# Kernel tuning notes

Hardware: AMD Instinct MI355X
Metric: run time of the kernel (lower is better)

Reference implementation:

```python
import jax, jax.numpy as jnp
import numpy as np

EPS = 1e-5
NEG = -10000.0


def rel_shift(x):
    # x: [B, H, T1, T2] with T2 = 2*T1 - 1 -> returns [B, H, T1, T1]
    B, H, T1, T2 = x.shape
    x = jnp.pad(x, ((0, 0), (0, 0), (0, 0), (1, 0)))        # [B,H,T1,T2+1]
    x = x.reshape(B, H, T2 + 1, T1)[:, :, 1:, :].reshape(B, H, T1, T2)
    return x[:, :, :, : T2 // 2 + 1]


def setup_inputs() -> dict:
    key = jax.random.key(0)
    B, C, T, H = 4, 512, 1024, 8
    ks = jax.random.split(key, 16)
    s = 0.02
    inp = {
        "x": jax.random.normal(ks[0], (B, C, T), jnp.float32),
        "pos_emb": jax.random.normal(ks[1], (1, C, 2 * T - 1), jnp.float32),
        "x_mask": jnp.ones((B, 1, T), jnp.float32),
        "gamma": jnp.ones((C,), jnp.float32),
        "beta": jnp.zeros((C,), jnp.float32),
        "Wq": jax.random.normal(ks[2], (C, C), jnp.float32) * s,
        "bq": jnp.zeros((C,), jnp.float32),
        "Wk": jax.random.normal(ks[3], (C, C), jnp.float32) * s,
        "bk": jnp.zeros((C,), jnp.float32),
        "Wv": jax.random.normal(ks[4], (C, C), jnp.float32) * s,
        "bv": jnp.zeros((C,), jnp.float32),
        "Wp": jax.random.normal(ks[5], (C, C), jnp.float32) * s,
        "u_bias": jax.random.normal(ks[6], (H, C // H), jnp.float32) * s,
        "v_bias": jax.random.normal(ks[7], (H, C // H), jnp.float32) * s,
        "Wo": jax.random.normal(ks[8], (C, C), jnp.float32) * s,
        "bo": jnp.zeros((C,), jnp.float32),
    }
    return inp


def reference(x, pos_emb, x_mask, gamma, beta, Wq, bq, Wk, bk, Wv, bv, Wp,
              u_bias, v_bias, Wo, bo):
    B, C, T = x.shape
    H, Dh = u_bias.shape

    # channel LayerNorm (axis=1)
    mean = jnp.mean(x, axis=1, keepdims=True)
    var = jnp.mean((x - mean) ** 2, axis=1, keepdims=True)
    xn = (x - mean) * jax.lax.rsqrt(var + EPS)
    xn = xn * gamma[None, :, None] + beta[None, :, None]

    conv1x1 = lambda W, b, z: jnp.einsum('oc,bct->bot', W, z) + b[None, :, None]
    q = conv1x1(Wq, bq, xn).reshape(B, H, Dh, T)
    k = conv1x1(Wk, bk, xn).reshape(B, H, Dh, T)
    v = conv1x1(Wv, bv, xn).reshape(B, H, Dh, T)
    p = jnp.einsum('oc,xct->xot', Wp, pos_emb)          # [1, C, 2T-1], no bias
    p = p.reshape(p.shape[0], H, Dh, -1)[0]             # [H, Dh, 2T-1]

    content = jnp.einsum('bhdt,bhds->bhts', q + u_bias[None, :, :, None], k)
    pos = jnp.einsum('bhdt,hds->bhts', q + v_bias[None, :, :, None], p)
    pos = rel_shift(pos)                                 # [B, H, T, T]

    score = (content + pos) / jnp.sqrt(jnp.float32(C))
    attn_mask = x_mask[:, :, None, :] * x_mask[:, :, :, None]  # [B,1,T,T]
    score = jnp.where(attn_mask == 0, NEG, score)
    attn = jax.nn.softmax(score, axis=-1)

    # context[d,t] = sum_s v[d,s] * attn[s,t]
    ctx = jnp.einsum('bhds,bhst->bhdt', v, attn).reshape(B, C, T)
    return jnp.einsum('oc,bct->bot', Wo, ctx) + bo[None, :, None]
```

## Files before the change

kernel.cpp:

```cpp
#include <hip/hip_runtime.h>
#include <hip/hip_bf16.h>
#include <cmath>

typedef unsigned short u16;
typedef __bf16 bf16_t;
typedef bf16_t bf16x8 __attribute__((ext_vector_type(8)));
typedef float f32x4 __attribute__((ext_vector_type(4)));
typedef u16 u16x8 __attribute__((ext_vector_type(8)));

#define MFMA16(A,B,C) __builtin_amdgcn_mfma_f32_16x16x32_bf16(A,B,C,0,0,0)

#define CB 512
#define TT 1024
#define NH 8
#define DH 64
#define ALPHA (0.044194173824159216f * 1.4426950408889634f)
#define MASKL 14426.950408889634f

static __device__ __forceinline__ u16 f2b(float f) {
  unsigned u = __float_as_uint(f);
  unsigned r = u + 0x7FFFu + ((u >> 16) & 1u);
  return (u16)(r >> 16);
}
static __device__ __forceinline__ float b2f(u16 u) {
  return __uint_as_float(((unsigned)u) << 16);
}
static __device__ __forceinline__ bf16x8 ldb8(const u16* p) {
  return *reinterpret_cast<const bf16x8*>(p);
}

__global__ __launch_bounds__(256)
void convert5(const float* __restrict__ Wq, const float* __restrict__ Wk,
              const float* __restrict__ Wv, const float* __restrict__ Wp,
              const float* __restrict__ Wo,
              u16* __restrict__ Wstk, u16* __restrict__ WoB)
{
  int i = blockIdx.x * 256 + threadIdx.x;
  int sel = i >> 15, loc = i & 32767;
  const float* src = (sel == 0) ? Wq : (sel == 1) ? Wk : (sel == 2) ? Wv
                   : (sel == 3) ? Wp : Wo;
  const float4 a = ((const float4*)src)[loc * 2 + 0];
  const float4 b = ((const float4*)src)[loc * 2 + 1];
  u16x8 o;
  o[0] = f2b(a.x); o[1] = f2b(a.y); o[2] = f2b(a.z); o[3] = f2b(a.w);
  o[4] = f2b(b.x); o[5] = f2b(b.y); o[6] = f2b(b.z); o[7] = f2b(b.w);
  u16* dst = (sel < 4) ? (Wstk + (size_t)i * 8) : (WoB + (size_t)loc * 8);
  *(u16x8*)dst = o;
}

__global__ __launch_bounds__(256)
void transpose_pe(const float* __restrict__ pe, u16* __restrict__ posT)
{
  __shared__ float tile[64][65];
  int j0 = blockIdx.x * 64, c0 = blockIdx.y * 64;
  for (int e = threadIdx.x; e < 4096; e += 256) {
    int cc = e >> 6, jj = e & 63;
    int j = j0 + jj;
    tile[jj][cc] = (j < 2047) ? pe[(size_t)(c0 + cc) * 2047 + j] : 0.f;
  }
  __syncthreads();
  for (int e = threadIdx.x; e < 4096; e += 256) {
    int jj = e >> 6, cc = e & 63;
    posT[(size_t)(j0 + jj) * 512 + c0 + cc] = f2b(tile[jj][cc]);
  }
}

__global__ __launch_bounds__(256)
void ln_kernel(const float* __restrict__ x, const float* __restrict__ gamma,
               const float* __restrict__ beta, u16* __restrict__ xnT)
{
  __shared__ float sred[8][33], ssred[8][33];
  int tl = threadIdx.x & 31, cg = threadIdx.x >> 5;
  int t = blockIdx.x * 32 + tl;
  int b = blockIdx.y;
  const float* xb = x + (size_t)b * CB * TT + t;
  float s = 0.f, ss = 0.f;
  for (int c = cg * 64; c < cg * 64 + 64; ++c) {
    float v = xb[(size_t)c * TT];
    s += v; ss += v * v;
  }
  sred[cg][tl] = s; ssred[cg][tl] = ss;
  __syncthreads();
  float S = 0.f, SS = 0.f;
  #pragma unroll
  for (int g = 0; g < 8; ++g) { S += sred[g][tl]; SS += ssred[g][tl]; }
  float mean = S * (1.f / 512.f);
  float var = SS * (1.f / 512.f) - mean * mean;
  float rstd = rsqrtf(var + 1e-5f);
  u16* orow = xnT + ((size_t)b * TT + t) * CB;
  for (int c8 = 0; c8 < 8; ++c8) {
    int c = cg * 64 + c8 * 8;
    u16x8 o;
    #pragma unroll
    for (int j = 0; j < 8; ++j) {
      float v = xb[(size_t)(c + j) * TT];
      o[j] = f2b((v - mean) * rstd * gamma[c + j] + beta[c + j]);
    }
    *(u16x8*)(orow + c) = o;
  }
}

template<int K, int OMODE>
__global__ __launch_bounds__(256)
void gemm2(const u16* __restrict__ A, const u16* __restrict__ XT,
           long xStride, long oStride, int Nout,
           const float* __restrict__ b0, void* __restrict__ outv)
{
  const int tid = threadIdx.x, w = tid >> 6, lane = tid & 63;
  const int ln16 = lane & 15, kg = lane >> 4;
  const int wm = w & 1, wn = w >> 1;
  const int m0 = blockIdx.y * 64 + wm * 32;
  const int n0 = blockIdx.x * 128 + wn * 64;
  const int z = blockIdx.z;
  const u16* Ar = A + (size_t)(m0 + ln16) * K + kg * 8;
  const u16* Br = XT + (size_t)z * xStride + (size_t)(n0 + ln16) * K + kg * 8;
  f32x4 acc[2][4] = {};
  #pragma unroll 2
  for (int ks = 0; ks < K / 32; ++ks) {
    bf16x8 a[2], bb[4];
    #pragma unroll
    for (int mt = 0; mt < 2; ++mt) a[mt] = ldb8(Ar + (size_t)mt * 16 * K + ks * 32);
    #pragma unroll
    for (int nt = 0; nt < 4; ++nt) bb[nt] = ldb8(Br + (size_t)nt * 16 * K + ks * 32);
    #pragma unroll
    for (int mt = 0; mt < 2; ++mt)
      #pragma unroll
      for (int nt = 0; nt < 4; ++nt)
        acc[mt][nt] = MFMA16(a[mt], bb[nt], acc[mt][nt]);
  }
  float add[2][4];
  #pragma unroll
  for (int mt = 0; mt < 2; ++mt)
    #pragma unroll
    for (int jr = 0; jr < 4; ++jr)
      add[mt][jr] = b0 ? b0[m0 + mt * 16 + kg * 4 + jr] : 0.f;
  #pragma unroll
  for (int mt = 0; mt < 2; ++mt)
    #pragma unroll
    for (int nt = 0; nt < 4; ++nt) {
      const int n = n0 + nt * 16 + ln16;
      if constexpr (OMODE == 0) {
        float* out = (float*)outv;
        #pragma unroll
        for (int jr = 0; jr < 4; ++jr)
          out[(size_t)z * oStride + (size_t)(m0 + mt * 16 + kg * 4 + jr) * Nout + n] =
              acc[mt][nt][jr] + add[mt][jr];
      } else {
        const int m_low = m0 + mt * 16;
        const size_t o = (size_t)z * oStride +
                         ((size_t)(m_low >> 6) * Nout + n) * 64 + (m_low & 63) + kg * 4;
        ushort4 s4;
        s4.x = f2b(acc[mt][nt][0] + add[mt][0]);
        s4.y = f2b(acc[mt][nt][1] + add[mt][1]);
        s4.z = f2b(acc[mt][nt][2] + add[mt][2]);
        s4.w = f2b(acc[mt][nt][3] + add[mt][3]);
        *reinterpret_cast<ushort4*>((u16*)outv + o) = s4;
      }
    }
}

__global__ __launch_bounds__(256)
void proj_qkv2(const u16* __restrict__ Wstk, const u16* __restrict__ xnT,
               const float* __restrict__ bq, const float* __restrict__ ub,
               const float* __restrict__ bk, const float* __restrict__ bv,
               u16* __restrict__ quB, u16* __restrict__ kB, u16* __restrict__ vB)
{
  const int tid = threadIdx.x, w = tid >> 6, lane = tid & 63;
  const int ln16 = lane & 15, kg = lane >> 4;
  const int wm = w & 1, wn = w >> 1;
  const int my = blockIdx.y;
  const int sec = my >> 3;
  const int m0l = (my & 7) * 64 + wm * 32;
  const int n0 = blockIdx.x * 128 + wn * 64;
  const int z = blockIdx.z;
  const long XS = (long)TT * CB;
  const long QS = (long)NH * TT * DH;
  const u16* Ar = Wstk + (size_t)(sec * 512 + m0l + ln16) * 512 + kg * 8;
  const u16* Br = xnT + (size_t)z * XS + (size_t)(n0 + ln16) * 512 + kg * 8;
  f32x4 acc[2][4] = {};
  #pragma unroll 2
  for (int ks = 0; ks < 16; ++ks) {
    bf16x8 a[2], bb[4];
    #pragma unroll
    for (int mt = 0; mt < 2; ++mt) a[mt] = ldb8(Ar + (size_t)mt * 16 * 512 + ks * 32);
    #pragma unroll
    for (int nt = 0; nt < 4; ++nt) bb[nt] = ldb8(Br + (size_t)nt * 16 * 512 + ks * 32);
    #pragma unroll
    for (int mt = 0; mt < 2; ++mt)
      #pragma unroll
      for (int nt = 0; nt < 4; ++nt)
        acc[mt][nt] = MFMA16(a[mt], bb[nt], acc[mt][nt]);
  }
  const float scl = (sec == 0) ? ALPHA : 1.f;
  float add[2][4];
  #pragma unroll
  for (int mt = 0; mt < 2; ++mt)
    #pragma unroll
    for (int jr = 0; jr < 4; ++jr) {
      int m = m0l + mt * 16 + kg * 4 + jr;
      add[mt][jr] = (sec == 0) ? (bq[m] + ub[m]) : (sec == 1) ? bk[m] : bv[m];
    }
  if (sec < 2) {
    u16* dst = sec ? kB : quB;
    #pragma unroll
    for (int mt = 0; mt < 2; ++mt)
      #pragma unroll
      for (int nt = 0; nt < 4; ++nt) {
        const int n = n0 + nt * 16 + ln16;
        const int m_low = m0l + mt * 16;
        const size_t o = (size_t)z * QS +
                         ((size_t)(m_low >> 6) * TT + n) * 64 + (m_low & 63) + kg * 4;
        ushort4 s4;
        s4.x = f2b((acc[mt][nt][0] + add[mt][0]) * scl);
        s4.y = f2b((acc[mt][nt][1] + add[mt][1]) * scl);
        s4.z = f2b((acc[mt][nt][2] + add[mt][2]) * scl);
        s4.w = f2b((acc[mt][nt][3] + add[mt][3]) * scl);
        *reinterpret_cast<ushort4*>(dst + o) = s4;
      }
  } else {
    #pragma unroll
    for (int mt = 0; mt < 2; ++mt)
      #pragma unroll
      for (int nt = 0; nt < 4; ++nt) {
        const int n = n0 + nt * 16 + ln16;
        #pragma unroll
        for (int jr = 0; jr < 4; ++jr)
          vB[(size_t)z * QS + (size_t)(m0l + mt * 16 + kg * 4 + jr) * TT + n] =
              f2b(acc[mt][nt][jr] + add[mt][jr]);
      }
  }
}

__global__ __launch_bounds__(256)
void corr_kernel(const u16* __restrict__ pp, const float* __restrict__ ub,
                 const float* __restrict__ vb, float* __restrict__ corr)
{
  const int h = blockIdx.y;
  const int j = blockIdx.x * 256 + threadIdx.x;
  __shared__ float dl[64];
  if (threadIdx.x < 64)
    dl[threadIdx.x] = vb[h * 64 + threadIdx.x] - ub[h * 64 + threadIdx.x];
  __syncthreads();
  const u16* prow = pp + ((size_t)h * 2048 + j) * 64;
  float s = 0.f;
  #pragma unroll
  for (int d8 = 0; d8 < 8; ++d8) {
    union { bf16x8 v; u16 u[8]; } pu;
    pu.v = ldb8(prow + d8 * 8);
    #pragma unroll
    for (int e = 0; e < 8; ++e) s += b2f(pu.u[e]) * dl[d8 * 8 + e];
  }
  corr[h * 2048 + j] = s * ALPHA;
}

__global__ __launch_bounds__(256)
void stats_mfma(const u16* __restrict__ qu, const u16* __restrict__ kk_,
                const u16* __restrict__ pp, const float* __restrict__ corr,
                const float* __restrict__ xmask, float* __restrict__ ls)
{
  const int tid = threadIdx.x;
  const int w = tid >> 6, lane = tid & 63;
  const int ln16 = lane & 15, kg = lane >> 4;
  const int bid = blockIdx.x;
  const int bh = (bid & 7) + 8 * ((bid >> 3) & 3);
  const int rest = bid >> 5;
  const int qi0 = (rest & 31) * 32;
  const int part = rest >> 5;
  const int b = bh >> 3, h = bh & 7;
  const u16* quP = qu + (size_t)bh * TT * DH;
  const u16* kP  = kk_ + (size_t)bh * TT * DH;
  const u16* pP  = pp + (size_t)h * 2048 * DH;
  const float* corrP = corr + (h << 11);

  __shared__ u16 G[4][32][100];
  __shared__ float red[4][32];

  bf16x8 qa[2][2];
  #pragma unroll
  for (int mt = 0; mt < 2; ++mt)
    #pragma unroll
    for (int kc = 0; kc < 2; ++kc)
      qa[mt][kc] = ldb8(&quP[(size_t)(qi0 + mt * 16 + ln16) * DH + kc * 32 + kg * 8]);
  float aq[2][4];
  #pragma unroll
  for (int mt = 0; mt < 2; ++mt)
    #pragma unroll
    for (int jr = 0; jr < 4; ++jr)
      aq[mt][jr] = (xmask[b * TT + qi0 + mt * 16 + kg * 4 + jr] - 1.f) * MASKL;

  float rs[2][4] = {};
  for (int c = 0; c < 2; ++c) {
    const int ki0 = (part * 8 + c * 4 + w) * 64;
    const int j0 = ki0 - qi0 + 992;
    #pragma unroll
    for (int nt = 0; nt < 6; ++nt) {
      const size_t po = (size_t)(j0 + nt * 16 + ln16) * DH + kg * 8;
      bf16x8 pb0 = ldb8(&pP[po]);
      bf16x8 pb1 = ldb8(&pP[po + 32]);
      const float cval = corrP[j0 + nt * 16 + ln16];
      #pragma unroll
      for (int mt = 0; mt < 2; ++mt) {
        f32x4 g = {0.f, 0.f, 0.f, 0.f};
        g = MFMA16(qa[mt][0], pb0, g);
        g = MFMA16(qa[mt][1], pb1, g);
        #pragma unroll
        for (int jr = 0; jr < 4; ++jr)
          G[w][mt * 16 + kg * 4 + jr][nt * 16 + ln16] = f2b(g[jr] + cval);
      }
    }
    #pragma unroll
    for (int nt = 0; nt < 4; ++nt) {
      const size_t ko = (size_t)(ki0 + nt * 16 + ln16) * DH + kg * 8;
      bf16x8 kb0 = ldb8(&kP[ko]);
      bf16x8 kb1 = ldb8(&kP[ko + 32]);
      const float ak = (xmask[b * TT + ki0 + nt * 16 + ln16] - 1.f) * MASKL;
      #pragma unroll
      for (int mt = 0; mt < 2; ++mt) {
        f32x4 dd = { aq[mt][0] + ak, aq[mt][1] + ak, aq[mt][2] + ak, aq[mt][3] + ak };
        dd = MFMA16(qa[mt][0], kb0, dd);
        dd = MFMA16(qa[mt][1], kb1, dd);
        #pragma unroll
        for (int jr = 0; jr < 4; ++jr) {
          const int qrow = mt * 16 + kg * 4 + jr;
          const int u = nt * 16 + ln16 - qrow + 31;
          rs[mt][jr] += exp2f(dd[jr] + b2f(G[w][qrow][u]));
        }
      }
    }
  }
  #pragma unroll
  for (int mt = 0; mt < 2; ++mt)
    #pragma unroll
    for (int jr = 0; jr < 4; ++jr) {
      float v = rs[mt][jr];
      v += __shfl_xor(v, 1); v += __shfl_xor(v, 2);
      v += __shfl_xor(v, 4); v += __shfl_xor(v, 8);
      rs[mt][jr] = v;
    }
  if (ln16 == 0) {
    #pragma unroll
    for (int mt = 0; mt < 2; ++mt)
      #pragma unroll
      for (int jr = 0; jr < 4; ++jr)
        red[w][mt * 16 + kg * 4 + jr] = rs[mt][jr];
  }
  __syncthreads();
  if (tid < 32)
    ls[(size_t)part * 32768 + (size_t)bh * TT + qi0 + tid] =
        red[0][tid] + red[1][tid] + red[2][tid] + red[3][tid];
}

__global__ __launch_bounds__(256)
void vscale(u16* __restrict__ vv, const float* __restrict__ ls)
{
  int i = blockIdx.x * 256 + threadIdx.x;
  int bh = i >> 13;
  int rem = i & 8191;
  int d = rem >> 7;
  int qi0 = (rem & 127) * 8;
  const float* lsP = ls + bh * 1024 + qi0;
  u16* row = vv + ((size_t)bh * 64 + d) * 1024 + qi0;
  union { u16x8 v; u16 u[8]; } t;
  t.v = *(u16x8*)row;
  u16x8 o;
  #pragma unroll
  for (int e = 0; e < 8; ++e) {
    float linv = __builtin_amdgcn_rcpf(lsP[e] + lsP[32768 + e]);
    o[e] = f2b(b2f(t.u[e]) * linv);
  }
  *(u16x8*)row = o;
}

__global__ __launch_bounds__(256)
void ctx_mfma(const u16* __restrict__ qu, const u16* __restrict__ kk_,
              const u16* __restrict__ vv, const u16* __restrict__ pp,
              const float* __restrict__ corr, const float* __restrict__ xmask,
              u16* __restrict__ ctx2)
{
  const int tid = threadIdx.x;
  const int w = tid >> 6, lane = tid & 63;
  const int ln16 = lane & 15, kg = lane >> 4;
  const int bid = blockIdx.x;
  const int bh = (bid & 7) + 8 * ((bid >> 3) & 3);
  const int rest = bid >> 5;
  const int t0 = (rest & 15) * 64;
  const int part = rest >> 4;
  const int b = bh >> 3, h = bh & 7;
  const u16* quP = qu + (size_t)bh * TT * DH;
  const u16* kP  = kk_ + (size_t)bh * TT * DH;
  const u16* vP  = vv + (size_t)bh * DH * TT;
  const u16* pP  = pp + (size_t)h * 2048 * DH;
  const float* corrP = corr + (h << 11);

  __shared__ u16 G[4][16][84];
  __shared__ __align__(16) u16 P[64][72];

  bf16x8 ka[4][2];
  #pragma unroll
  for (int nt = 0; nt < 4; ++nt)
    #pragma unroll
    for (int kc = 0; kc < 2; ++kc)
      ka[nt][kc] = ldb8(&kP[(size_t)(t0 + nt * 16 + ln16) * DH + kc * 32 + kg * 8]);
  float at4[4];
  #pragma unroll
  for (int nt = 0; nt < 4; ++nt)
    at4[nt] = (xmask[b * TT + t0 + nt * 16 + ln16] - 1.f) * MASKL;

  f32x4 cacc[4] = {};
  for (int qc = part * 4; qc < part * 4 + 4; ++qc) {
    const int qw = qc * 64 + w * 16;
    const int j0 = t0 - qw + 1008;
    const size_t qo = (size_t)(qw + ln16) * DH + kg * 8;
    bf16x8 qa0 = ldb8(&quP[qo]), qa1 = ldb8(&quP[qo + 32]);
    #pragma unroll
    for (int nt = 0; nt < 5; ++nt) {
      const size_t po = (size_t)(j0 + nt * 16 + ln16) * DH + kg * 8;
      bf16x8 pb0 = ldb8(&pP[po]), pb1 = ldb8(&pP[po + 32]);
      const float cval = corrP[j0 + nt * 16 + ln16];
      f32x4 g = {0.f, 0.f, 0.f, 0.f};
      g = MFMA16(qa0, pb0, g);
      g = MFMA16(qa1, pb1, g);
      #pragma unroll
      for (int jr = 0; jr < 4; ++jr)
        G[w][kg * 4 + jr][nt * 16 + ln16] = f2b(g[jr] + cval);
    }
    float aqv[4];
    #pragma unroll
    for (int jr = 0; jr < 4; ++jr)
      aqv[jr] = (xmask[b * TT + qw + kg * 4 + jr] - 1.f) * MASKL;
    __syncthreads();
    #pragma unroll
    for (int nt = 0; nt < 4; ++nt) {
      f32x4 dd = { aqv[0] + at4[nt], aqv[1] + at4[nt],
                   aqv[2] + at4[nt], aqv[3] + at4[nt] };
      dd = MFMA16(qa0, ka[nt][0], dd);
      dd = MFMA16(qa1, ka[nt][1], dd);
      unsigned lo = 0, hi = 0;
      #pragma unroll
      for (int jr = 0; jr < 4; ++jr) {
        const int qrow = kg * 4 + jr;
        const int u = nt * 16 + ln16 - qrow + 15;
        const float e = exp2f(dd[jr] + b2f(G[w][qrow][u]));
        const unsigned bb = f2b(e);
        if (jr == 0) lo = bb; else if (jr == 1) lo |= bb << 16;
        else if (jr == 2) hi = bb; else hi |= bb << 16;
      }
      *reinterpret_cast<uint2*>(&P[nt * 16 + ln16][w * 16 + kg * 4]) = make_uint2(lo, hi);
    }
    __syncthreads();
    const size_t vbase = (size_t)(w * 16 + ln16) * TT + qc * 64 + kg * 8;
    bf16x8 vf0 = ldb8(&vP[vbase]), vf1 = ldb8(&vP[vbase + 32]);
    #pragma unroll
    for (int nt = 0; nt < 4; ++nt) {
      bf16x8 pb0 = *reinterpret_cast<const bf16x8*>(&P[nt * 16 + ln16][kg * 8]);
      bf16x8 pb1 = *reinterpret_cast<const bf16x8*>(&P[nt * 16 + ln16][32 + kg * 8]);
      cacc[nt] = MFMA16(vf0, pb0, cacc[nt]);
      cacc[nt] = MFMA16(vf1, pb1, cacc[nt]);
    }
  }
  #pragma unroll
  for (int nt = 0; nt < 4; ++nt) {
    const int t = t0 + nt * 16 + ln16;
    ushort4 s4;
    s4.x = f2b(cacc[nt][0]); s4.y = f2b(cacc[nt][1]);
    s4.z = f2b(cacc[nt][2]); s4.w = f2b(cacc[nt][3]);
    *reinterpret_cast<ushort4*>(
      &ctx2[((size_t)b * TT + t) * 2048 + part * 512 + h * 64 + w * 16 + kg * 4]) = s4;
  }
}

__global__ __launch_bounds__(256)
void reduce_ctx(const u16* __restrict__ ctx2, u16* __restrict__ ctxS)
{
  int i = blockIdx.x * 256 + threadIdx.x;
  int row = i >> 6;
  int c0 = (i & 63) * 8;
  const u16* src = ctx2 + (size_t)row * 2048 + c0;
  float s[8] = {};
  #pragma unroll
  for (int p = 0; p < 4; ++p) {
    union { u16x8 v; u16 u[8]; } t;
    t.v = *(const u16x8*)(src + p * 512);
    #pragma unroll
    for (int e = 0; e < 8; ++e) s[e] += b2f(t.u[e]);
  }
  u16x8 o;
  #pragma unroll
  for (int e = 0; e < 8; ++e) o[e] = f2b(s[e]);
  *(u16x8*)(ctxS + (size_t)row * 512 + c0) = o;
}

extern "C" void kernel_launch(void* const* d_in, const int* in_sizes, int n_in,
                              void* d_out, int out_size, void* d_ws, size_t ws_size,
                              hipStream_t stream)
{
  (void)in_sizes; (void)n_in; (void)out_size;
  const float* x     = (const float*)d_in[0];
  const float* pe    = (const float*)d_in[1];
  const float* xm    = (const float*)d_in[2];
  const float* gamma = (const float*)d_in[3];
  const float* beta  = (const float*)d_in[4];
  const float* Wq    = (const float*)d_in[5];
  const float* bq    = (const float*)d_in[6];
  const float* Wk    = (const float*)d_in[7];
  const float* bk    = (const float*)d_in[8];
  const float* Wv    = (const float*)d_in[9];
  const float* bv    = (const float*)d_in[10];
  const float* Wp    = (const float*)d_in[11];
  const float* ub    = (const float*)d_in[12];
  const float* vb    = (const float*)d_in[13];
  const float* Wo    = (const float*)d_in[14];
  const float* bo    = (const float*)d_in[15];

  char* ws = (char*)d_ws;
  u16*  quB  = (u16*) (ws + 0);
  u16*  ctxS = (u16*) (ws + 0);
  u16*  kB   = (u16*) (ws + 4194304);
  u16*  vB   = (u16*) (ws + 8388608);
  u16*  pB   = (u16*) (ws + 12582912);
  float* corrB = (float*)(ws + 14680064);
  float* lsB = (float*)(ws + 14745600);
  u16*  WoB  = (u16*) (ws + 15007744);
  u16*  ctx2 = (u16*) (ws + 15532032);
  u16*  xnT  = (u16*) (ws + 15532032);
  u16*  posT = (u16*) (ws + 19726336);
  u16*  Wstk = (u16*) (ws + 21823488);
  if (ws_size < 32309248) return;

  dim3 blk(256);

  convert5<<<dim3(640), blk, 0, stream>>>(Wq, Wk, Wv, Wp, Wo, Wstk, WoB);
  transpose_pe<<<dim3(32, 8), blk, 0, stream>>>(pe, posT);
  ln_kernel<<<dim3(32, 4), blk, 0, stream>>>(x, gamma, beta, xnT);

  proj_qkv2<<<dim3(8, 24, 4), blk, 0, stream>>>(Wstk, xnT, bq, ub, bk, bv, quB, kB, vB);
  gemm2<512, 1><<<dim3(16, 8, 1), blk, 0, stream>>>(
      Wstk + (size_t)1536 * 512, posT, 0, 0, 2048, nullptr, pB);
  corr_kernel<<<dim3(8, 8), blk, 0, stream>>>(pB, ub, vb, corrB);

  stats_mfma<<<dim3(2048), blk, 0, stream>>>(quB, kB, pB, corrB, xm, lsB);
  vscale<<<dim3(1024), blk, 0, stream>>>(vB, lsB);
  ctx_mfma<<<dim3(2048), blk, 0, stream>>>(quB, kB, vB, pB, corrB, xm, ctx2);
  reduce_ctx<<<dim3(1024), blk, 0, stream>>>(ctx2, ctxS);

  gemm2<512, 0><<<dim3(8, 8, 4), blk, 0, stream>>>(
      WoB, ctxS, (long)TT * CB, (long)CB * TT, TT, bo, (float*)d_out);
}
```

Before: 210.9 us.

## Replace LDS rel-shift staging with lane shuffles and double-buffer the P tile

```diff
diff --git a/kernel.cpp b/kernel.cpp
--- a/kernel.cpp
+++ b/kernel.cpp
@@ -261,6 +261,7 @@
   const int tid = threadIdx.x;
   const int w = tid >> 6, lane = tid & 63;
   const int ln16 = lane & 15, kg = lane >> 4;
+  const int l48 = lane & 48;
   const int bid = blockIdx.x;
   const int bh = (bid & 7) + 8 * ((bid >> 3) & 3);
   const int rest = bid >> 5;
@@ -272,7 +273,6 @@
   const u16* pP  = pp + (size_t)h * 2048 * DH;
   const float* corrP = corr + (h << 11);
 
-  __shared__ u16 G[4][32][100];
   __shared__ float red[4][32];
 
   bf16x8 qa[2][2];
@@ -293,37 +293,44 @@
     const int ki0 = (part * 8 + c * 4 + w) * 64;
     const int j0 = ki0 - qi0 + 992;
     #pragma unroll
-    for (int nt = 0; nt < 6; ++nt) {
-      const size_t po = (size_t)(j0 + nt * 16 + ln16) * DH + kg * 8;
-      bf16x8 pb0 = ldb8(&pP[po]);
-      bf16x8 pb1 = ldb8(&pP[po + 32]);
-      const float cval = corrP[j0 + nt * 16 + ln16];
-      #pragma unroll
-      for (int mt = 0; mt < 2; ++mt) {
-        f32x4 g = {0.f, 0.f, 0.f, 0.f};
-        g = MFMA16(qa[mt][0], pb0, g);
-        g = MFMA16(qa[mt][1], pb1, g);
+    for (int mt = 0; mt < 2; ++mt) {
+      f32x4 g[6];
+      #pragma unroll
+      for (int n = 0; n < 6; ++n) {
+        const size_t po = (size_t)(j0 + n * 16 + ln16) * DH + kg * 8;
+        bf16x8 pb0 = ldb8(&pP[po]);
+        bf16x8 pb1 = ldb8(&pP[po + 32]);
+        const float cval = corrP[j0 + n * 16 + ln16];
+        f32x4 t = {cval, cval, cval, cval};
+        t = MFMA16(qa[mt][0], pb0, t);
+        t = MFMA16(qa[mt][1], pb1, t);
+        g[n] = t;
+      }
+      f32x4 dd[4];
+      #pragma unroll
+      for (int nt = 0; nt < 4; ++nt) {
+        const size_t ko = (size_t)(ki0 + nt * 16 + ln16) * DH + kg * 8;
+        bf16x8 kb0 = ldb8(&kP[ko]);
+        bf16x8 kb1 = ldb8(&kP[ko + 32]);
+        const float ak = (xmask[b * TT + ki0 + nt * 16 + ln16] - 1.f) * MASKL;
+        f32x4 t = { aq[mt][0] + ak, aq[mt][1] + ak, aq[mt][2] + ak, aq[mt][3] + ak };
+        t = MFMA16(qa[mt][0], kb0, t);
+        t = MFMA16(qa[mt][1], kb1, t);
+        dd[nt] = t;
+      }
+      #pragma unroll
+      for (int jr = 0; jr < 4; ++jr) {
+        const int qrow = mt * 16 + kg * 4 + jr;
+        const int sh = ln16 + 31 - qrow;
+        const int src = l48 | (sh & 15);
+        const int o = sh >> 4;
+        float s[6];
         #pragma unroll
-        for (int jr = 0; jr < 4; ++jr)
-          G[w][mt * 16 + kg * 4 + jr][nt * 16 + ln16] = f2b(g[jr] + cval);
-      }
-    }
-    #pragma unroll
-    for (int nt = 0; nt < 4; ++nt) {
-      const size_t ko = (size_t)(ki0 + nt * 16 + ln16) * DH + kg * 8;
-      bf16x8 kb0 = ldb8(&kP[ko]);
-      bf16x8 kb1 = ldb8(&kP[ko + 32]);
-      const float ak = (xmask[b * TT + ki0 + nt * 16 + ln16] - 1.f) * MASKL;
-      #pragma unroll
-      for (int mt = 0; mt < 2; ++mt) {
-        f32x4 dd = { aq[mt][0] + ak, aq[mt][1] + ak, aq[mt][2] + ak, aq[mt][3] + ak };
-        dd = MFMA16(qa[mt][0], kb0, dd);
-        dd = MFMA16(qa[mt][1], kb1, dd);
+        for (int n = 0; n < 6; ++n) s[n] = __shfl(g[n][jr], src);
         #pragma unroll
-        for (int jr = 0; jr < 4; ++jr) {
-          const int qrow = mt * 16 + kg * 4 + jr;
-          const int u = nt * 16 + ln16 - qrow + 31;
-          rs[mt][jr] += exp2f(dd[jr] + b2f(G[w][qrow][u]));
+        for (int nt = 0; nt < 4; ++nt) {
+          const float val = (o == 0) ? s[nt] : (o == 1) ? s[nt + 1] : s[nt + 2];
+          rs[mt][jr] += exp2f(dd[nt][jr] + val);
         }
       }
     }
@@ -351,27 +358,6 @@
 }
 
 __global__ __launch_bounds__(256)
-void vscale(u16* __restrict__ vv, const float* __restrict__ ls)
-{
-  int i = blockIdx.x * 256 + threadIdx.x;
-  int bh = i >> 13;
-  int rem = i & 8191;
-  int d = rem >> 7;
-  int qi0 = (rem & 127) * 8;
-  const float* lsP = ls + bh * 1024 + qi0;
-  u16* row = vv + ((size_t)bh * 64 + d) * 1024 + qi0;
-  union { u16x8 v; u16 u[8]; } t;
-  t.v = *(u16x8*)row;
-  u16x8 o;
-  #pragma unroll
-  for (int e = 0; e < 8; ++e) {
-    float linv = __builtin_amdgcn_rcpf(lsP[e] + lsP[32768 + e]);
-    o[e] = f2b(b2f(t.u[e]) * linv);
-  }
-  *(u16x8*)row = o;
-}
-
-__global__ __launch_bounds__(256)
 void ctx_mfma(const u16* __restrict__ qu, const u16* __restrict__ kk_,
               const u16* __restrict__ vv, const u16* __restrict__ pp,
               const float* __restrict__ corr, const float* __restrict__ xmask,
@@ -380,6 +366,7 @@
   const int tid = threadIdx.x;
   const int w = tid >> 6, lane = tid & 63;
   const int ln16 = lane & 15, kg = lane >> 4;
+  const int l48 = lane & 48;
   const int bid = blockIdx.x;
   const int bh = (bid & 7) + 8 * ((bid >> 3) & 3);
   const int rest = bid >> 5;
@@ -392,8 +379,7 @@
   const u16* pP  = pp + (size_t)h * 2048 * DH;
   const float* corrP = corr + (h << 11);
 
-  __shared__ u16 G[4][16][84];
-  __shared__ __align__(16) u16 P[64][72];
+  __shared__ __align__(16) u16 P[2][64][72];
 
   bf16x8 ka[4][2];
   #pragma unroll
@@ -406,29 +392,34 @@
   for (int nt = 0; nt < 4; ++nt)
     at4[nt] = (xmask[b * TT + t0 + nt * 16 + ln16] - 1.f) * MASKL;
 
-  f32x4 cacc[4] = {};
-  for (int qc = part * 4; qc < part * 4 + 4; ++qc) {
-    const int qw = qc * 64 + w * 16;
+  auto scores = [&](int qcn, int buf) {
+    const int qw = qcn * 64 + w * 16;
     const int j0 = t0 - qw + 1008;
     const size_t qo = (size_t)(qw + ln16) * DH + kg * 8;
     bf16x8 qa0 = ldb8(&quP[qo]), qa1 = ldb8(&quP[qo + 32]);
-    #pragma unroll
-    for (int nt = 0; nt < 5; ++nt) {
-      const size_t po = (size_t)(j0 + nt * 16 + ln16) * DH + kg * 8;
+    f32x4 g[5];
+    #pragma unroll
+    for (int n = 0; n < 5; ++n) {
+      const size_t po = (size_t)(j0 + n * 16 + ln16) * DH + kg * 8;
       bf16x8 pb0 = ldb8(&pP[po]), pb1 = ldb8(&pP[po + 32]);
-      const float cval = corrP[j0 + nt * 16 + ln16];
-      f32x4 g = {0.f, 0.f, 0.f, 0.f};
-      g = MFMA16(qa0, pb0, g);
-      g = MFMA16(qa1, pb1, g);
-      #pragma unroll
-      for (int jr = 0; jr < 4; ++jr)
-        G[w][kg * 4 + jr][nt * 16 + ln16] = f2b(g[jr] + cval);
+      const float cval = corrP[j0 + n * 16 + ln16];
+      f32x4 t = {cval, cval, cval, cval};
+      t = MFMA16(qa0, pb0, t);
+      t = MFMA16(qa1, pb1, t);
+      g[n] = t;
+    }
+    float sg[4][5];
+    #pragma unroll
+    for (int jr = 0; jr < 4; ++jr) {
+      const int qrow = kg * 4 + jr;
+      const int src = l48 | ((ln16 + 15 - qrow) & 15);
+      #pragma unroll
+      for (int n = 0; n < 5; ++n) sg[jr][n] = __shfl(g[n][jr], src);
     }
     float aqv[4];
     #pragma unroll
     for (int jr = 0; jr < 4; ++jr)
       aqv[jr] = (xmask[b * TT + qw + kg * 4 + jr] - 1.f) * MASKL;
-    __syncthreads();
     #pragma unroll
     for (int nt = 0; nt < 4; ++nt) {
       f32x4 dd = { aqv[0] + at4[nt], aqv[1] + at4[nt],
@@ -439,23 +430,35 @@
       #pragma unroll
       for (int jr = 0; jr < 4; ++jr) {
         const int qrow = kg * 4 + jr;
-        const int u = nt * 16 + ln16 - qrow + 15;
-        const float e = exp2f(dd[jr] + b2f(G[w][qrow][u]));
+        const float val = (ln16 <= qrow) ? sg[jr][nt] : sg[jr][nt + 1];
+        const float e = exp2f(dd[jr] + val);
         const unsigned bb = f2b(e);
         if (jr == 0) lo = bb; else if (jr == 1) lo |= bb << 16;
         else if (jr == 2) hi = bb; else hi |= bb << 16;
       }
-      *reinterpret_cast<uint2*>(&P[nt * 16 + ln16][w * 16 + kg * 4]) = make_uint2(lo, hi);
-    }
-    __syncthreads();
+      *reinterpret_cast<uint2*>(&P[buf][nt * 16 + ln16][w * 16 + kg * 4]) =
+          make_uint2(lo, hi);
+    }
+  };
+
+  f32x4 cacc[4] = {};
+  scores(part * 4, 0);
+  __syncthreads();
+  #pragma unroll
+  for (int i = 0; i < 4; ++i) {
+    const int qc = part * 4 + i;
     const size_t vbase = (size_t)(w * 16 + ln16) * TT + qc * 64 + kg * 8;
     bf16x8 vf0 = ldb8(&vP[vbase]), vf1 = ldb8(&vP[vbase + 32]);
     #pragma unroll
     for (int nt = 0; nt < 4; ++nt) {
-      bf16x8 pb0 = *reinterpret_cast<const bf16x8*>(&P[nt * 16 + ln16][kg * 8]);
-      bf16x8 pb1 = *reinterpret_cast<const bf16x8*>(&P[nt * 16 + ln16][32 + kg * 8]);
+      bf16x8 pb0 = *reinterpret_cast<const bf16x8*>(&P[i & 1][nt * 16 + ln16][kg * 8]);
+      bf16x8 pb1 = *reinterpret_cast<const bf16x8*>(&P[i & 1][nt * 16 + ln16][32 + kg * 8]);
       cacc[nt] = MFMA16(vf0, pb0, cacc[nt]);
       cacc[nt] = MFMA16(vf1, pb1, cacc[nt]);
+    }
+    if (i < 3) {
+      scores(qc + 1, (i + 1) & 1);
+      __syncthreads();
     }
   }
   #pragma unroll
@@ -467,6 +470,27 @@
     *reinterpret_cast<ushort4*>(
       &ctx2[((size_t)b * TT + t) * 2048 + part * 512 + h * 64 + w * 16 + kg * 4]) = s4;
   }
+}
+
+__global__ __launch_bounds__(256)
+void vscale(u16* __restrict__ vv, const float* __restrict__ ls)
+{
+  int i = blockIdx.x * 256 + threadIdx.x;
+  int bh = i >> 13;
+  int rem = i & 8191;
+  int d = rem >> 7;
+  int qi0 = (rem & 127) * 8;
+  const float* lsP = ls + bh * 1024 + qi0;
+  u16* row = vv + ((size_t)bh * 64 + d) * 1024 + qi0;
+  union { u16x8 v; u16 u[8]; } t;
+  t.v = *(u16x8*)row;
+  u16x8 o;
+  #pragma unroll
+  for (int e = 0; e < 8; ++e) {
+    float linv = __builtin_amdgcn_rcpf(lsP[e] + lsP[32768 + e]);
+    o[e] = f2b(b2f(t.u[e]) * linv);
+  }
+  *(u16x8*)row = o;
 }
 
 __global__ __launch_bounds__(256)
```

New measurement: 233.9 us. 10.9% more time.
